# Optimization experiments

Measured on AMD Instinct MI355X. Metric: run time of the kernel, lower is better.

## Reference

```python
import jax, jax.numpy as jnp
import numpy as np

N, E, F, H, G, EPS = 50000, 500000, 128, 192, 256, 1e-5


def setup_inputs() -> dict:
    key = jax.random.key(0)
    ks = jax.random.split(key, 16)
    s = 0.05
    return {
        "x": jax.random.normal(ks[0], (N, F), jnp.float32),
        "edge_index": jax.random.randint(ks[1], (2, E), 0, N),
        "batch": jnp.sort(jax.random.randint(ks[2], (N,), 0, G)),
        "num_graphs": G,
        "w_rel0": jax.random.normal(ks[3], (H, F)) * s,
        "b_rel0": jnp.zeros((H,), jnp.float32),
        "w_root0": jax.random.normal(ks[4], (H, F)) * s,
        "w_rel": jax.random.normal(ks[5], (3, H, H)) * s,
        "b_rel": jnp.zeros((3, H), jnp.float32),
        "w_root": jax.random.normal(ks[6], (3, H, H)) * s,
        "bn_gamma": jnp.ones((4, H), jnp.float32),
        "bn_beta": jnp.zeros((4, H), jnp.float32),
        "head_w1": jax.random.normal(ks[7], (H, H)) * s,
        "head_b1": jnp.zeros((H,), jnp.float32),
        "head_w2": jax.random.normal(ks[8], (H, H)) * s,
        "head_b2": jnp.zeros((H,), jnp.float32),
        "out_w": jax.random.normal(ks[9], (1, H)) * s,
        "out_b": jnpp if False else jnp.zeros((1,), jnp.float32),
    }


def _conv_bn_relu(x, src, dst, n_nodes, wr, br, wroot, gamma, beta):
    # PyG GraphConv: out_i = lin_rel(sum_{j->i} x_j) + lin_root(x_i)
    agg = jax.ops.segment_sum(x[src], dst, num_segments=n_nodes)  # [N, d]
    h = agg @ wr.T + br + x @ wroot.T                             # [N, H]
    mu = h.mean(axis=0)
    var = h.var(axis=0)  # biased, as torch BN train mode
    h = (h - mu) * jax.lax.rsqrt(var + EPS) * gamma + beta
    return jax.nn.relu(h)


def reference(x, edge_index, batch, num_graphs, w_rel0, b_rel0, w_root0,
              w_rel, b_rel, w_root, bn_gamma, bn_beta,
              head_w1, head_b1, head_w2, head_b2, out_w, out_b):
    src, dst = edge_index[0], edge_index[1]
    n_nodes = x.shape[0]
    h = _conv_bn_relu(x, src, dst, n_nodes, w_rel0, b_rel0, w_root0,
                      bn_gamma[0], bn_beta[0])
    for i in range(3):
        h = _conv_bn_relu(h, src, dst, n_nodes, w_rel[i], b_rel[i], w_root[i],
                          bn_gamma[i + 1], bn_beta[i + 1])
    # global mean pool per graph
    sums = jax.ops.segment_sum(h, batch, num_segments=num_graphs)   # [G, H]
    cnts = jax.ops.segment_sum(jnp.ones((n_nodes,), h.dtype), batch,
                               num_segments=num_graphs)
    g = sums / jnp.maximum(cnts, 1.0)[:, None]
    # MLP head (dropout = eval) + output linear
    hh = jax.nn.relu(g @ head_w1.T + head_b1) @ head_w2.T + head_b2
    out = hh @ out_w.T + out_b                                      # [G, 1]
    return out[:, 0]
```

## Files before the change

### kernel.cpp

```cpp
#include <hip/hip_runtime.h>

#define HD 192
#define FD0 128
#define NG 256
#define BNEPS 1e-5f

#define STAT_S  1048576.0f
#define STAT_IS (1.0f / 1048576.0f)
#define QS  2048.0f
#define QIS (1.0f / 2048.0f)

typedef unsigned short u16;
typedef __attribute__((ext_vector_type(8))) short bf16x8;
typedef __attribute__((ext_vector_type(4))) float f32x4;

static inline int idiv(int a, int b) { return (a + b - 1) / b; }

__device__ __forceinline__ float b2f(u16 u) {
    unsigned int v = ((unsigned int)u) << 16;
    return __builtin_bit_cast(float, v);
}
__device__ __forceinline__ u16 f2b(float f) {
    unsigned int x = __builtin_bit_cast(unsigned int, f);
    return (u16)((x + 0x7FFFu + ((x >> 16) & 1u)) >> 16);
}
__device__ __forceinline__ short f2q(float v) {
    return (short)__float2int_rn(fmaxf(fminf(v, 15.9f), -15.9f) * QS);
}

__device__ __forceinline__ void async_cp16(const void* g, void* l) {
    __builtin_amdgcn_global_load_lds(
        (const __attribute__((address_space(1))) unsigned int*)g,
        (__attribute__((address_space(3))) unsigned int*)l, 16, 0, 0);
}

__global__ __launch_bounds__(256) void convert_x(const float* __restrict__ in,
    u16* __restrict__ xb, short* __restrict__ xq, int n4)
{
    const int i = blockIdx.x * 256 + threadIdx.x;
    if (i >= n4) return;
    const float4 v = ((const float4*)in)[i];
    u16 o[4] = { f2b(v.x), f2b(v.y), f2b(v.z), f2b(v.w) };
    ((ushort4*)xb)[i] = *(ushort4*)o;
    short q[4] = { f2q(v.x), f2q(v.y), f2q(v.z), f2q(v.w) };
    ((short4*)xq)[i] = *(short4*)q;
}

__global__ __launch_bounds__(256) void pack_weights(const float* __restrict__ wr,
    const float* __restrict__ wt, u16* __restrict__ out, int K)
{
    const int idx = blockIdx.x * 256 + threadIdx.x;
    const int total = HD * 2 * K;
    if (idx >= total) return;
    const int j  = idx & 7;
    const int t  = idx >> 3;
    const int c  = t & 15;
    const int kg = (t >> 4) & 3;
    const int rest = t >> 6;
    const int fglob = rest % 12;
    const int chunk = rest / 12;
    const int col = fglob * 16 + c;
    const int k   = chunk * 32 + kg * 8 + j;
    const float v = (k < K) ? wr[(size_t)col * K + k] : wt[(size_t)col * K + (k - K)];
    out[idx] = f2b(v);
}

__global__ __launch_bounds__(256) void transpose_w(const float* __restrict__ w,
                                                   float* __restrict__ wt)
{
    const int idx = blockIdx.x * 256 + threadIdx.x;
    if (idx >= HD * HD) return;
    const int t = idx % HD, k = idx / HD;
    wt[idx] = w[(size_t)t * HD + k];
}

__global__ __launch_bounds__(256) void hist_kernel(const int* __restrict__ dst,
                                                   int* __restrict__ deg, int E)
{
    const int e = blockIdx.x * 256 + threadIdx.x;
    if (e < E) atomicAdd(&deg[dst[e]], 1);
}

__global__ __launch_bounds__(256) void scan_partial(const int* __restrict__ deg,
                                                    int* __restrict__ psum, int N)
{
    __shared__ int s[256];
    const int t = threadIdx.x;
    const int i = blockIdx.x * 256 + t;
    s[t] = (i < N) ? deg[i] : 0;
    __syncthreads();
    for (int off = 128; off > 0; off >>= 1) {
        if (t < off) s[t] += s[t + off];
        __syncthreads();
    }
    if (t == 0) psum[blockIdx.x] = s[0];
}

__global__ __launch_bounds__(256) void scan_small(int* __restrict__ psum, int M)
{
    __shared__ int s[256];
    const int t = threadIdx.x;
    s[t] = (t < M) ? psum[t] : 0;
    __syncthreads();
    for (int off = 1; off < 256; off <<= 1) {
        const int u = (t >= off) ? s[t - off] : 0;
        __syncthreads();
        s[t] += u;
        __syncthreads();
    }
    if (t < M) psum[t] = (t == 0) ? 0 : s[t - 1];
}

__global__ __launch_bounds__(256) void scan_expand(const int* __restrict__ deg,
    const int* __restrict__ psum, int* __restrict__ rowptr, int N, int E)
{
    __shared__ int s[256];
    const int t = threadIdx.x;
    const int i = blockIdx.x * 256 + t;
    const int v = (i < N) ? deg[i] : 0;
    s[t] = v;
    __syncthreads();
    for (int off = 1; off < 256; off <<= 1) {
        const int u = (t >= off) ? s[t - off] : 0;
        __syncthreads();
        s[t] += u;
        __syncthreads();
    }
    if (i < N) rowptr[i] = psum[blockIdx.x] + s[t] - v;
    if (i == N - 1) rowptr[N] = E;
}

__global__ __launch_bounds__(256) void fill_kernel(const int* __restrict__ src,
    const int* __restrict__ dst, const int* __restrict__ rowptr,
    int* __restrict__ cursor, int* __restrict__ eidx, int E)
{
    const int e = blockIdx.x * 256 + threadIdx.x;
    if (e >= E) return;
    const int d = dst[e];
    const int p = atomicAdd(&cursor[d], 1);
    eidx[rowptr[d] + p] = src[e];
}

template<int FD>
__global__ __launch_bounds__(256) void gather_kernel(
    const short* __restrict__ hq, const int* __restrict__ rowptr,
    const int* __restrict__ eidx, u16* __restrict__ aggb, int N)
{
    constexpr int GW = FD / 32;
    constexpr int ND = GW / 2;
    const int lane = threadIdx.x & 63;
    const int half = lane >> 5;
    const int g    = lane & 31;
    const int n    = blockIdx.x * 4 + (threadIdx.x >> 6);
    if (n >= N) return;
    const int beg = rowptr[n], end = rowptr[n + 1];

    int acc[GW];
#pragma unroll
    for (int i = 0; i < GW; ++i) acc[i] = 0;

    int j = beg + half;
    for (; j + 6 < end; j += 8) {
        const int s0 = eidx[j],     s1 = eidx[j + 2];
        const int s2 = eidx[j + 4], s3 = eidx[j + 6];
        const unsigned int* p0 = (const unsigned int*)(hq + (size_t)s0 * FD + g * GW);
        const unsigned int* p1 = (const unsigned int*)(hq + (size_t)s1 * FD + g * GW);
        const unsigned int* p2 = (const unsigned int*)(hq + (size_t)s2 * FD + g * GW);
        const unsigned int* p3 = (const unsigned int*)(hq + (size_t)s3 * FD + g * GW);
        unsigned int u0[ND], u1[ND], u2[ND], u3[ND];
#pragma unroll
        for (int d = 0; d < ND; ++d) { u0[d] = p0[d]; u1[d] = p1[d]; u2[d] = p2[d]; u3[d] = p3[d]; }
#pragma unroll
        for (int d = 0; d < ND; ++d) {
            acc[2*d]   += (int)(short)(u0[d] & 0xffffu) + (int)(short)(u1[d] & 0xffffu)
                        + (int)(short)(u2[d] & 0xffffu) + (int)(short)(u3[d] & 0xffffu);
            acc[2*d+1] += (((int)u0[d]) >> 16) + (((int)u1[d]) >> 16)
                        + (((int)u2[d]) >> 16) + (((int)u3[d]) >> 16);
        }
    }
    for (; j < end; j += 2) {
        const int s0 = eidx[j];
        const unsigned int* p0 = (const unsigned int*)(hq + (size_t)s0 * FD + g * GW);
#pragma unroll
        for (int d = 0; d < ND; ++d) {
            const unsigned int u = p0[d];
            acc[2*d]   += (int)(short)(u & 0xffffu);
            acc[2*d+1] += ((int)u) >> 16;
        }
    }
#pragma unroll
    for (int i = 0; i < GW; ++i) acc[i] += __shfl_xor(acc[i], 32);

    if (half == 0) {
        unsigned int* q = (unsigned int*)(aggb + (size_t)n * FD + g * GW);
#pragma unroll
        for (int d = 0; d < ND; ++d) {
            const u16 lo = f2b((float)acc[2*d]   * QIS);
            const u16 hi = f2b((float)acc[2*d+1] * QIS);
            q[d] = (unsigned int)lo | ((unsigned int)hi << 16);
        }
    }
}

template<int K1, int K2>
__global__ __launch_bounds__(512, 1) void gemm_mfma(
    const u16* __restrict__ A1, const u16* __restrict__ A2,
    const u16* __restrict__ Wb, const float* __restrict__ bias,
    u16* __restrict__ Hout, long long* __restrict__ statsq, int N)
{
    constexpr int KC  = K1 + K2;
    constexpr int NC  = KC / 32;
    constexpr int NC1 = K1 / 32;
    __shared__ u16 bsh[HD * KC];

    const int tid  = threadIdx.x;
    const int wave = tid >> 6, lane = tid & 63;
    const int c = lane & 15, kg = lane >> 4;
    const int row0 = blockIdx.x * 256 + wave * 32;

    {
        constexpr int NST = (HD * KC) / (512 * 8);
        const u16* wsrc = Wb + tid * 8;
        u16* ldst = bsh + tid * 8;
#pragma unroll
        for (int i = 0; i < NST; ++i)
            async_cp16(wsrc + i * 4096, ldst + i * 4096);
    }

    int arc[2];
#pragma unroll
    for (int m = 0; m < 2; ++m) {
        const int r = row0 + m * 16 + c;
        arc[m] = r < N ? r : N - 1;
    }

    f32x4 acc[2][12];
#pragma unroll
    for (int m = 0; m < 2; ++m)
#pragma unroll
        for (int f = 0; f < 12; ++f) acc[m][f] = (f32x4){0.f, 0.f, 0.f, 0.f};

    __syncthreads();

    for (int ch = 0; ch < NC; ++ch) {
        const int kk = ch * 32;
        bf16x8 a[2];
#pragma unroll
        for (int m = 0; m < 2; ++m) {
            const u16* p = (ch < NC1) ? (A1 + (size_t)arc[m] * K1 + kk + kg * 8)
                                      : (A2 + (size_t)arc[m] * K2 + (kk - K1) + kg * 8);
            a[m] = *(const bf16x8*)p;
        }
#pragma unroll
        for (int f = 0; f < 12; ++f) {
            const bf16x8 b = *(const bf16x8*)&bsh[ch * 6144 + f * 512 + kg * 128 + c * 8];
            acc[0][f] = __builtin_amdgcn_mfma_f32_16x16x32_bf16(a[0], b, acc[0][f], 0, 0, 0);
            acc[1][f] = __builtin_amdgcn_mfma_f32_16x16x32_bf16(a[1], b, acc[1][f], 0, 0, 0);
        }
    }

    float s1v[12], s2v[12];
#pragma unroll
    for (int f = 0; f < 12; ++f) { s1v[f] = 0.f; s2v[f] = 0.f; }

#pragma unroll
    for (int f = 0; f < 12; ++f) {
        const int col = f * 16 + c;
        const float bv = bias[col];
#pragma unroll
        for (int m = 0; m < 2; ++m)
#pragma unroll
            for (int r = 0; r < 4; ++r) {
                const int orow = row0 + m * 16 + kg * 4 + r;
                if (orow < N) {
                    const float v = acc[m][f][r] + bv;
                    s1v[f] += v;
                    s2v[f] += v * v;
                    Hout[(size_t)orow * HD + col] = f2b(v);
                }
            }
    }
#pragma unroll
    for (int f = 0; f < 12; ++f) {
        s1v[f] += __shfl_xor(s1v[f], 16); s1v[f] += __shfl_xor(s1v[f], 32);
        s2v[f] += __shfl_xor(s2v[f], 16); s2v[f] += __shfl_xor(s2v[f], 32);
    }
    __syncthreads();
    float* red = (float*)bsh;
    if (kg == 0) {
#pragma unroll
        for (int f = 0; f < 12; ++f) {
            red[wave * HD + f * 16 + c]            = s1v[f];
            red[8 * HD + wave * HD + f * 16 + c]   = s2v[f];
        }
    }
    __syncthreads();
    if (tid < HD) {
        float a1 = 0.f, a2 = 0.f;
#pragma unroll
        for (int w = 0; w < 8; ++w) {
            a1 += red[w * HD + tid];
            a2 += red[8 * HD + w * HD + tid];
        }
        atomicAdd((unsigned long long*)&statsq[tid],
                  (unsigned long long)(long long)llrintf(a1 * STAT_S));
        atomicAdd((unsigned long long*)&statsq[HD + tid],
                  (unsigned long long)(long long)llrintf(a2 * STAT_S));
    }
}

__global__ __launch_bounds__(256) void norm_relu(const u16* __restrict__ hpre,
    u16* __restrict__ hb, short* __restrict__ hq,
    const long long* __restrict__ statsq,
    const float* __restrict__ gamma, const float* __restrict__ beta, int N)
{
    __shared__ float sc[HD], sh[HD];
    const int t = threadIdx.x;
    if (t < HD) {
        const float inv = 1.0f / (float)N;
        const float sum = (float)statsq[t] * STAT_IS;
        const float sq  = (float)statsq[HD + t] * STAT_IS;
        const float mu  = sum * inv;
        const float var = sq * inv - mu * mu;
        const float s   = gamma[t] * rsqrtf(var + BNEPS);
        sc[t] = s; sh[t] = beta[t] - mu * s;
    }
    __syncthreads();
    const int idx = blockIdx.x * 256 + t;
    const int total = N * (HD / 8);
    if (idx >= total) return;
    const int c8 = idx % (HD / 8);
    uint4 packed = ((const uint4*)hpre)[idx];
    const u16* pu = (const u16*)&packed;
    u16 ob[8]; short oq[8];
#pragma unroll
    for (int j = 0; j < 8; ++j) {
        const int cc = c8 * 8 + j;
        const float v = fmaxf(0.f, fmaf(b2f(pu[j]), sc[cc], sh[cc]));
        ob[j] = f2b(v);
        oq[j] = (short)__float2int_rn(fminf(v, 15.9f) * QS);
    }
    ((uint4*)hb)[idx] = *(uint4*)ob;
    ((uint4*)hq)[idx] = *(uint4*)oq;
}

__global__ __launch_bounds__(256) void pool_head_kernel(
    const u16* __restrict__ h, const int* __restrict__ batch, int N,
    const float* __restrict__ w1t, const float* __restrict__ b1,
    const float* __restrict__ w2t, const float* __restrict__ b2,
    const float* __restrict__ ow, const float* __restrict__ ob,
    float* __restrict__ out)
{
    __shared__ float pp[8][HD];
    __shared__ float gv[HD];
    __shared__ float h1[HD];
    __shared__ float h2[HD];
    const int g = blockIdx.x;
    const int t = threadIdx.x;
    const int rp = t >> 5;
    const int o  = t & 31;

    int lo = 0, hi = N;
    while (lo < hi) { int m = (lo + hi) >> 1; if (batch[m] < g) lo = m + 1; else hi = m; }
    const int start = lo;
    hi = N;
    while (lo < hi) { int m = (lo + hi) >> 1; if (batch[m] < g + 1) lo = m + 1; else hi = m; }
    const int end = lo;

    float facc[8];
#pragma unroll
    for (int i = 0; i < 8; ++i) facc[i] = 0.f;
    if (o < 24) {
        for (int r = start + rp; r < end; r += 8) {
            const uint4 pv = *(const uint4*)(h + (size_t)r * HD + o * 8);
            const u16* pu = (const u16*)&pv;
#pragma unroll
            for (int i = 0; i < 8; ++i) facc[i] += b2f(pu[i]);
        }
#pragma unroll
        for (int i = 0; i < 8; ++i) pp[rp][o * 8 + i] = facc[i];
    }
    __syncthreads();
    if (t < HD) {
        float s = 0.f;
#pragma unroll
        for (int r = 0; r < 8; ++r) s += pp[r][t];
        gv[t] = s / fmaxf((float)(end - start), 1.0f);
    }
    __syncthreads();
    if (t < HD) {
        float acc = b1[t];
#pragma unroll 4
        for (int k = 0; k < HD; ++k)
            acc = fmaf(gv[k], w1t[k * HD + t], acc);
        h1[t] = fmaxf(acc, 0.f);
    }
    __syncthreads();
    if (t < HD) {
        float acc = b2[t];
#pragma unroll 4
        for (int k = 0; k < HD; ++k)
            acc = fmaf(h1[k], w2t[k * HD + t], acc);
        h2[t] = acc * ow[t];
    }
    __syncthreads();
    if (t < 64) {
        float s = h2[t] + h2[t + 64] + h2[t + 128];
#pragma unroll
        for (int d = 1; d < 64; d <<= 1) s += __shfl_xor(s, d);
        if (t == 0) out[g] = s + ob[0];
    }
}

extern "C" void kernel_launch(void* const* d_in, const int* in_sizes, int n_in,
                              void* d_out, int out_size, void* d_ws, size_t ws_size,
                              hipStream_t stream)
{
    const float* x       = (const float*)d_in[0];
    const int*   ei      = (const int*)d_in[1];
    const int*   batch   = (const int*)d_in[2];
    const float* w_rel0  = (const float*)d_in[4];
    const float* b_rel0  = (const float*)d_in[5];
    const float* w_root0 = (const float*)d_in[6];
    const float* w_rel   = (const float*)d_in[7];
    const float* b_rel   = (const float*)d_in[8];
    const float* w_root  = (const float*)d_in[9];
    const float* bn_g    = (const float*)d_in[10];
    const float* bn_b    = (const float*)d_in[11];
    const float* hw1     = (const float*)d_in[12];
    const float* hb1     = (const float*)d_in[13];
    const float* hw2     = (const float*)d_in[14];
    const float* hb2     = (const float*)d_in[15];
    const float* ow      = (const float*)d_in[16];
    const float* ob      = (const float*)d_in[17];
    float* out = (float*)d_out;

    const int N = in_sizes[0] / FD0;
    const int E = in_sizes[1] / 2;
    const int* src = ei;
    const int* dst = ei + E;
    const int M = idiv(N, 256);

    char* ws = (char*)d_ws;
    size_t off = 0;
    u16*   xb   = (u16*)(ws + off);   off += (size_t)N * FD0 * 2;
    short* xq   = (short*)(ws + off); off += (size_t)N * FD0 * 2;
    u16*   hb   = (u16*)(ws + off);   off += (size_t)N * HD * 2;
    short* hq   = (short*)(ws + off); off += (size_t)N * HD * 2;
    u16*   aggb = (u16*)(ws + off);   off += (size_t)N * HD * 2;
    u16*   hpre = (u16*)(ws + off);   off += (size_t)N * HD * 2;
    u16*   wp0  = (u16*)(ws + off);   off += (size_t)HD * 2 * FD0 * 2;
    u16*   wp123= (u16*)(ws + off);   off += (size_t)3 * HD * 2 * HD * 2;
    off = (off + 15) & ~(size_t)15;
    float* w1t = (float*)(ws + off); off += (size_t)HD * HD * 4;
    float* w2t = (float*)(ws + off); off += (size_t)HD * HD * 4;
    long long* statsq = (long long*)(ws + off); off += 2 * HD * sizeof(long long);
    int*   rowptr = (int*)(ws + off); off += (size_t)(N + 1) * 4;
    int*   deg    = (int*)(ws + off); off += (size_t)N * 4;
    int*   psum   = (int*)(ws + off); off += (size_t)M * 4;
    int*   eidx   = (int*)(ws + off); off += (size_t)E * 4;

    const dim3 b256(256), b512(512);

    convert_x<<<idiv(N * FD0 / 4, 256), b256, 0, stream>>>(x, xb, xq, N * FD0 / 4);
    pack_weights<<<idiv(HD * 2 * FD0, 256), b256, 0, stream>>>(w_rel0, w_root0, wp0, FD0);
    for (int i = 0; i < 3; ++i)
        pack_weights<<<idiv(HD * 2 * HD, 256), b256, 0, stream>>>(
            w_rel + (size_t)i * HD * HD, w_root + (size_t)i * HD * HD,
            wp123 + (size_t)i * HD * 2 * HD, HD);
    transpose_w<<<idiv(HD * HD, 256), b256, 0, stream>>>(hw1, w1t);
    transpose_w<<<idiv(HD * HD, 256), b256, 0, stream>>>(hw2, w2t);
    hipMemsetAsync(deg, 0, (size_t)N * sizeof(int), stream);
    hist_kernel<<<idiv(E, 256), b256, 0, stream>>>(dst, deg, E);
    scan_partial<<<M, b256, 0, stream>>>(deg, psum, N);
    scan_small<<<1, b256, 0, stream>>>(psum, M);
    scan_expand<<<M, b256, 0, stream>>>(deg, psum, rowptr, N, E);
    hipMemsetAsync(deg, 0, (size_t)N * sizeof(int), stream);
    fill_kernel<<<idiv(E, 256), b256, 0, stream>>>(src, dst, rowptr, deg, eidx, E);

    hipMemsetAsync(statsq, 0, 2 * HD * sizeof(long long), stream);
    gather_kernel<FD0><<<idiv(N, 4), b256, 0, stream>>>(xq, rowptr, eidx, aggb, N);
    gemm_mfma<FD0, FD0><<<idiv(N, 256), b512, 0, stream>>>(aggb, xb, wp0, b_rel0,
                                                           hpre, statsq, N);
    norm_relu<<<idiv(N * (HD / 8), 256), b256, 0, stream>>>(hpre, hb, hq, statsq,
                                                            bn_g, bn_b, N);

    for (int i = 0; i < 3; ++i) {
        hipMemsetAsync(statsq, 0, 2 * HD * sizeof(long long), stream);
        gather_kernel<HD><<<idiv(N, 4), b256, 0, stream>>>(hq, rowptr, eidx, aggb, N);
        gemm_mfma<HD, HD><<<idiv(N, 256), b512, 0, stream>>>(
            aggb, hb, wp123 + (size_t)i * HD * 2 * HD,
            b_rel + (size_t)i * HD, hpre, statsq, N);
        norm_relu<<<idiv(N * (HD / 8), 256), b256, 0, stream>>>(hpre, hb, hq, statsq,
            bn_g + (size_t)(i + 1) * HD, bn_b + (size_t)(i + 1) * HD, N);
    }

    pool_head_kernel<<<NG, b256, 0, stream>>>(hb, batch, N, w1t, hb1, w2t, hb2,
                                              ow, ob, out);
}
```

Baseline: 405.4 us.

## Merge setup kernels, batch stats memsets, and split pooling into parallel partial pass

```diff
diff --git a/kernel.cpp b/kernel.cpp
--- a/kernel.cpp
+++ b/kernel.cpp
@@ -9,6 +9,8 @@
 #define STAT_IS (1.0f / 1048576.0f)
 #define QS  2048.0f
 #define QIS (1.0f / 2048.0f)
+#define POOL_S  65536.0f
+#define POOL_IS (1.0f / 65536.0f)
 
 typedef unsigned short u16;
 typedef __attribute__((ext_vector_type(8))) short bf16x8;
@@ -46,12 +48,9 @@
     ((short4*)xq)[i] = *(short4*)q;
 }
 
-__global__ __launch_bounds__(256) void pack_weights(const float* __restrict__ wr,
-    const float* __restrict__ wt, u16* __restrict__ out, int K)
-{
-    const int idx = blockIdx.x * 256 + threadIdx.x;
-    const int total = HD * 2 * K;
-    if (idx >= total) return;
+__device__ __forceinline__ void pack_one(const float* __restrict__ wr,
+    const float* __restrict__ wt, u16* __restrict__ out, int K, int idx)
+{
     const int j  = idx & 7;
     const int t  = idx >> 3;
     const int c  = t & 15;
@@ -65,13 +64,35 @@
     out[idx] = f2b(v);
 }
 
-__global__ __launch_bounds__(256) void transpose_w(const float* __restrict__ w,
-                                                   float* __restrict__ wt)
-{
-    const int idx = blockIdx.x * 256 + threadIdx.x;
+__global__ __launch_bounds__(256) void pack_all(const float* __restrict__ wr0,
+    const float* __restrict__ wt0, const float* __restrict__ w_rel,
+    const float* __restrict__ w_root, u16* __restrict__ wp0,
+    u16* __restrict__ wp123)
+{
+    const int T0 = HD * 2 * FD0;
+    const int T1 = HD * 2 * HD;
+    int idx = blockIdx.x * 256 + threadIdx.x;
+    if (idx < T0) {
+        pack_one(wr0, wt0, wp0, FD0, idx);
+    } else {
+        idx -= T0;
+        if (idx >= 3 * T1) return;
+        const int li = idx / T1;
+        const int r  = idx - li * T1;
+        pack_one(w_rel + (size_t)li * HD * HD, w_root + (size_t)li * HD * HD,
+                 wp123 + (size_t)li * T1, HD, r);
+    }
+}
+
+__global__ __launch_bounds__(256) void transpose_all(const float* __restrict__ w1,
+    const float* __restrict__ w2, float* __restrict__ w1t, float* __restrict__ w2t)
+{
+    int idx = blockIdx.x * 256 + threadIdx.x;
+    const float* w = w1; float* o = w1t;
+    if (idx >= HD * HD) { idx -= HD * HD; w = w2; o = w2t; }
     if (idx >= HD * HD) return;
     const int t = idx % HD, k = idx / HD;
-    wt[idx] = w[(size_t)t * HD + k];
+    o[idx] = w[(size_t)t * HD + k];
 }
 
 __global__ __launch_bounds__(256) void hist_kernel(const int* __restrict__ dst,
@@ -344,21 +365,58 @@
     ((uint4*)hq)[idx] = *(uint4*)oq;
 }
 
-__global__ __launch_bounds__(256) void pool_head_kernel(
-    const u16* __restrict__ h, const int* __restrict__ batch, int N,
+__global__ __launch_bounds__(192) void pool_partial(const u16* __restrict__ hb,
+    const int* __restrict__ batch, int* __restrict__ gsumq, int N)
+{
+    const int t   = threadIdx.x;
+    const int rl  = t / 24;
+    const int oct = t % 24;
+    const int r0  = blockIdx.x * 256;
+    const int rend = (r0 + 256 < N) ? r0 + 256 : N;
+
+    float facc[8];
+#pragma unroll
+    for (int i = 0; i < 8; ++i) facc[i] = 0.f;
+    int cur = -1;
+
+    for (int r = r0 + rl; r < rend; r += 8) {
+        const int b = batch[r];
+        if (b != cur) {
+            if (cur >= 0) {
+                int* q = gsumq + (size_t)cur * HD + oct * 8;
+#pragma unroll
+                for (int i = 0; i < 8; ++i)
+                    atomicAdd(&q[i], __float2int_rn(facc[i] * POOL_S));
+            }
+#pragma unroll
+            for (int i = 0; i < 8; ++i) facc[i] = 0.f;
+            cur = b;
+        }
+        const uint4 pv = *(const uint4*)(hb + (size_t)r * HD + oct * 8);
+        const u16* pu = (const u16*)&pv;
+#pragma unroll
+        for (int i = 0; i < 8; ++i) facc[i] += b2f(pu[i]);
+    }
+    if (cur >= 0) {
+        int* q = gsumq + (size_t)cur * HD + oct * 8;
+#pragma unroll
+        for (int i = 0; i < 8; ++i)
+            atomicAdd(&q[i], __float2int_rn(facc[i] * POOL_S));
+    }
+}
+
+__global__ __launch_bounds__(192) void head_kernel(
+    const int* __restrict__ gsumq, const int* __restrict__ batch, int N,
     const float* __restrict__ w1t, const float* __restrict__ b1,
     const float* __restrict__ w2t, const float* __restrict__ b2,
     const float* __restrict__ ow, const float* __restrict__ ob,
     float* __restrict__ out)
 {
-    __shared__ float pp[8][HD];
     __shared__ float gv[HD];
     __shared__ float h1[HD];
     __shared__ float h2[HD];
     const int g = blockIdx.x;
     const int t = threadIdx.x;
-    const int rp = t >> 5;
-    const int o  = t & 31;
 
     int lo = 0, hi = N;
     while (lo < hi) { int m = (lo + hi) >> 1; if (batch[m] < g) lo = m + 1; else hi = m; }
@@ -366,29 +424,11 @@
     hi = N;
     while (lo < hi) { int m = (lo + hi) >> 1; if (batch[m] < g + 1) lo = m + 1; else hi = m; }
     const int end = lo;
-
-    float facc[8];
-#pragma unroll
-    for (int i = 0; i < 8; ++i) facc[i] = 0.f;
-    if (o < 24) {
-        for (int r = start + rp; r < end; r += 8) {
-            const uint4 pv = *(const uint4*)(h + (size_t)r * HD + o * 8);
-            const u16* pu = (const u16*)&pv;
-#pragma unroll
-            for (int i = 0; i < 8; ++i) facc[i] += b2f(pu[i]);
-        }
-#pragma unroll
-        for (int i = 0; i < 8; ++i) pp[rp][o * 8 + i] = facc[i];
-    }
-    __syncthreads();
-    if (t < HD) {
-        float s = 0.f;
-#pragma unroll
-        for (int r = 0; r < 8; ++r) s += pp[r][t];
-        gv[t] = s / fmaxf((float)(end - start), 1.0f);
-    }
-    __syncthreads();
-    if (t < HD) {
+    const float cnt = fmaxf((float)(end - start), 1.0f);
+
+    gv[t] = (float)gsumq[(size_t)g * HD + t] * POOL_IS / cnt;
+    __syncthreads();
+    {
         float acc = b1[t];
 #pragma unroll 4
         for (int k = 0; k < HD; ++k)
@@ -396,7 +436,7 @@
         h1[t] = fmaxf(acc, 0.f);
     }
     __syncthreads();
-    if (t < HD) {
+    {
         float acc = b2[t];
 #pragma unroll 4
         for (int k = 0; k < HD; ++k)
@@ -454,22 +494,21 @@
     off = (off + 15) & ~(size_t)15;
     float* w1t = (float*)(ws + off); off += (size_t)HD * HD * 4;
     float* w2t = (float*)(ws + off); off += (size_t)HD * HD * 4;
-    long long* statsq = (long long*)(ws + off); off += 2 * HD * sizeof(long long);
+    long long* statsq4 = (long long*)(ws + off); off += 4 * 2 * HD * sizeof(long long);
+    int*   gsumq  = (int*)(ws + off); off += (size_t)NG * HD * 4;
     int*   rowptr = (int*)(ws + off); off += (size_t)(N + 1) * 4;
     int*   deg    = (int*)(ws + off); off += (size_t)N * 4;
     int*   psum   = (int*)(ws + off); off += (size_t)M * 4;
     int*   eidx   = (int*)(ws + off); off += (size_t)E * 4;
 
-    const dim3 b256(256), b512(512);
+    const dim3 b256(256), b512(512), b192(192);
 
     convert_x<<<idiv(N * FD0 / 4, 256), b256, 0, stream>>>(x, xb, xq, N * FD0 / 4);
-    pack_weights<<<idiv(HD * 2 * FD0, 256), b256, 0, stream>>>(w_rel0, w_root0, wp0, FD0);
-    for (int i = 0; i < 3; ++i)
-        pack_weights<<<idiv(HD * 2 * HD, 256), b256, 0, stream>>>(
-            w_rel + (size_t)i * HD * HD, w_root + (size_t)i * HD * HD,
-            wp123 + (size_t)i * HD * 2 * HD, HD);
-    transpose_w<<<idiv(HD * HD, 256), b256, 0, stream>>>(hw1, w1t);
-    transpose_w<<<idiv(HD * HD, 256), b256, 0, stream>>>(hw2, w2t);
+    pack_all<<<idiv(HD * 2 * FD0 + 3 * HD * 2 * HD, 256), b256, 0, stream>>>(
+        w_rel0, w_root0, w_rel, w_root, wp0, wp123);
+    transpose_all<<<idiv(2 * HD * HD, 256), b256, 0, stream>>>(hw1, hw2, w1t, w2t);
+    hipMemsetAsync(statsq4, 0, 4 * 2 * HD * sizeof(long long) + (size_t)NG * HD * 4,
+                   stream);
     hipMemsetAsync(deg, 0, (size_t)N * sizeof(int), stream);
     hist_kernel<<<idiv(E, 256), b256, 0, stream>>>(dst, deg, E);
     scan_partial<<<M, b256, 0, stream>>>(deg, psum, N);
@@ -478,15 +517,14 @@
     hipMemsetAsync(deg, 0, (size_t)N * sizeof(int), stream);
     fill_kernel<<<idiv(E, 256), b256, 0, stream>>>(src, dst, rowptr, deg, eidx, E);
 
-    hipMemsetAsync(statsq, 0, 2 * HD * sizeof(long long), stream);
     gather_kernel<FD0><<<idiv(N, 4), b256, 0, stream>>>(xq, rowptr, eidx, aggb, N);
     gemm_mfma<FD0, FD0><<<idiv(N, 256), b512, 0, stream>>>(aggb, xb, wp0, b_rel0,
-                                                           hpre, statsq, N);
-    norm_relu<<<idiv(N * (HD / 8), 256), b256, 0, stream>>>(hpre, hb, hq, statsq,
+                                                           hpre, statsq4, N);
+    norm_relu<<<idiv(N * (HD / 8), 256), b256, 0, stream>>>(hpre, hb, hq, statsq4,
                                                             bn_g, bn_b, N);
 
     for (int i = 0; i < 3; ++i) {
-        hipMemsetAsync(statsq, 0, 2 * HD * sizeof(long long), stream);
+        long long* statsq = statsq4 + (size_t)(i + 1) * 2 * HD;
         gather_kernel<HD><<<idiv(N, 4), b256, 0, stream>>>(hq, rowptr, eidx, aggb, N);
         gemm_mfma<HD, HD><<<idiv(N, 256), b512, 0, stream>>>(
             aggb, hb, wp123 + (size_t)i * HD * 2 * HD,
@@ -495,6 +533,7 @@
             bn_g + (size_t)(i + 1) * HD, bn_b + (size_t)(i + 1) * HD, N);
     }
 
-    pool_head_kernel<<<NG, b256, 0, stream>>>(hb, batch, N, w1t, hb1, w2t, hb2,
-                                              ow, ob, out);
-}
+    pool_partial<<<idiv(N, 256), b192, 0, stream>>>(hb, batch, gsumq, N);
+    head_kernel<<<NG, b192, 0, stream>>>(gsumq, batch, N, w1t, hb1, w2t, hb2,
+                                         ow, ob, out);
+}
```

New measurement: 418.6 us. 3.3% more time.
